# Optimization experiments

Hardware: AMD Instinct MI355X
Metric: run time of the kernel (lower is better)

Reference implementation:

```python
import jax, jax.numpy as jnp
import numpy as np

NHID = 128; NUM_CLASSES = 128; NUM_CONVS = 3; EDGE_RATIO = 0.8
B_GRAPHS = 256; N_PER_G = 256; E_PER_G = 512
N_TOTAL = B_GRAPHS * N_PER_G; E_TOTAL = B_GRAPHS * E_PER_G
ATOM_DIMS = [119, 4, 12, 12, 10, 6, 6, 2, 2]
BOND_DIMS = [5, 6, 2]


def setup_inputs():
    key = jax.random.key(0)
    ks = jax.random.split(key, 32)
    a_off = np.concatenate([[0], np.cumsum(ATOM_DIMS)[:-1]])
    x_idx = jnp.stack([jax.random.randint(ks[i], (N_TOTAL,), 0, dm) + int(o)
                       for i, (dm, o) in enumerate(zip(ATOM_DIMS, a_off))], axis=1)
    b_off = np.concatenate([[0], np.cumsum(BOND_DIMS)[:-1]])
    edge_attr_idx = jnp.stack([jax.random.randint(ks[9 + i], (E_TOTAL,), 0, dm) + int(o)
                               for i, (dm, o) in enumerate(zip(BOND_DIMS, b_off))], axis=1)
    # block-structured edges: each graph's edges are contiguous, endpoints local
    src = jax.random.randint(ks[12], (B_GRAPHS, E_PER_G), 0, N_PER_G)
    dst = jax.random.randint(ks[13], (B_GRAPHS, E_PER_G), 0, N_PER_G)
    off = jnp.arange(B_GRAPHS)[:, None] * N_PER_G
    edge_index = jnp.stack([(src + off).reshape(-1), (dst + off).reshape(-1)])
    batch = jnp.repeat(jnp.arange(B_GRAPHS), N_PER_G)
    s = 0.05
    d = NHID
    def rn(k, shape):
        return jax.random.normal(k, shape, dtype=jnp.float32) * s
    return {
        "x_idx": x_idx, "edge_attr_idx": edge_attr_idx,
        "edge_index": edge_index, "batch": batch,
        "atom_table": rn(ks[14], (sum(ATOM_DIMS), d)),
        "bond_table": rn(ks[15], (sum(BOND_DIMS), d)),
        "W_gcn": rn(ks[16], (NUM_CONVS, d, d)), "b_gcn": rn(ks[17], (NUM_CONVS, d)),
        "root_emb": rn(ks[18], (NUM_CONVS, d)),
        "W_hyp": rn(ks[19], (NUM_CONVS - 1, d, d)), "b_hyp": rn(ks[20], (NUM_CONVS - 1, d)),
        "W_sc": rn(ks[21], (NUM_CONVS - 1, d, 1)), "b_sc": rn(ks[22], (NUM_CONVS - 1, 1)),
        "Wc1": rn(ks[23], (3 * d, d)), "bc1": rn(ks[24], (d,)),
        "Wc2": rn(ks[25], (d, d // 2)), "bc2": rn(ks[26], (d // 2,)),
        "Wc3": rn(ks[27], (d // 2, NUM_CLASSES)), "bc3": rn(ks[28], (NUM_CLASSES,)),
    }


def reference(x_idx, edge_attr_idx, edge_index, batch, atom_table, bond_table,
              W_gcn, b_gcn, root_emb, W_hyp, b_hyp, W_sc, b_sc,
              Wc1, bc1, Wc2, bc2, Wc3, bc3):
    seg = jax.ops.segment_sum
    x = atom_table[x_idx].sum(axis=1)          # [N, d] AtomEncoder: sum of per-feature embeddings
    e = bond_table[edge_attr_idx].sum(axis=1)  # [E, d] BondEncoder
    edge_weight = None
    xs = 0.0
    for l in range(NUM_CONVS):
        E = edge_index.shape[1]
        # ---- DHT: dual hypergraph (edges -> nodes, nodes -> hyperedges), with loops & degree-1 mask
        flat = edge_index.T.reshape(-1)  # [2E] node ids in (src,dst,src,dst,...) order
        node_idx = jnp.concatenate([jnp.repeat(jnp.arange(E), 2), jnp.arange(E)])       # [3E]
        hyper_idx = jnp.concatenate([flat, N_TOTAL + jnp.arange(E)])                    # [3E]
        bc = seg(jnp.ones(2 * E, jnp.float32), flat, num_segments=N_TOTAL)
        mask = jnp.concatenate([bc[flat] != 1.0, jnp.ones((E,), dtype=bool)])
        w = mask.astype(x.dtype)
        NH = N_TOTAL + E
        # ---- GCNConv_OGB
        row, col = edge_index[0], edge_index[1]
        h = x @ W_gcn[l] + b_gcn[l]
        deg = seg(jnp.ones(E, x.dtype), row, num_segments=N_TOTAL) + 1.0
        dis = deg ** -0.5
        msg = (dis[row] * dis[col])[:, None] * jax.nn.relu(h[row] + e)
        if edge_weight is not None:
            msg = msg * edge_weight[:, None]
        x = jax.nn.relu(seg(msg, col, num_segments=N_TOTAL)
                        + jax.nn.relu(h + root_emb[l]) / deg[:, None])
        if l < NUM_CONVS - 1:
            # ---- HypergraphConv on edge features (nodes of dual = original edges)
            Dn = seg(w, node_idx, num_segments=E)
            Bh = seg(w, hyper_idx, num_segments=NH)
            Dinv = jnp.where(Dn > 0, 1.0 / Dn, 0.0)
            Binv = jnp.where(Bh > 0, 1.0 / Bh, 0.0)
            def hconv(feat, W, b):
                z = feat @ W
                m = seg(z[node_idx] * w[:, None], hyper_idx, num_segments=NH) * Binv[:, None]
                return seg(m[hyper_idx] * w[:, None], node_idx, num_segments=E) * Dinv[:, None] + b
            e = jax.nn.relu(hconv(e, W_hyp[l], b_hyp[l]))
            score = jnp.tanh(hconv(e, W_sc[l], b_sc[l]).squeeze(-1))  # [E]
            # ---- topk edge pooling (uniform per-graph blocks -> static k)
            Eg = E // B_GRAPHS
            k = int(np.ceil(EDGE_RATIO * Eg))
            _, loc = jax.lax.top_k(score.reshape(B_GRAPHS, Eg), k)
            perm = (loc + jnp.arange(B_GRAPHS)[:, None] * Eg).reshape(-1)
            edge_index = edge_index[:, perm]
            e = e[perm]
            edge_weight = jnp.clip(score[perm], 0.0, 1.0)
        # ---- readout: gmp | gap | gsp  (uniform graphs -> reshape)
        xr = x.reshape(B_GRAPHS, N_PER_G, NHID)
        xs = xs + jnp.concatenate([xr.max(axis=1), xr.mean(axis=1), xr.sum(axis=1)], axis=1)
    # ---- classifier (eval mode: dropout is identity)
    h1 = jax.nn.relu(xs @ Wc1 + bc1)
    h2 = jax.nn.relu(h1 @ Wc2 + bc2)
    return h2 @ Wc3 + bc3
```

## Files before the change

### kernel.cpp

```cpp
#include <hip/hip_runtime.h>
#include <hip/hip_bf16.h>
#include <math.h>

constexpr int NTOT = 65536;
constexpr int D    = 128;
constexpr int BG   = 256;
constexpr int E0 = 131072, E1 = 104960, E2 = 83968;
constexpr int EG0 = 512;
constexpr int KP0 = 410, KP1 = 328;

typedef __bf16 bf16x8 __attribute__((ext_vector_type(8)));
typedef __bf16 bf16x4 __attribute__((ext_vector_type(4)));
typedef __bf16 bf16x2 __attribute__((ext_vector_type(2)));
typedef float  f32x4  __attribute__((ext_vector_type(4)));

__device__ __forceinline__ float2 tof2(bf16x2 v) {
  return make_float2((float)v[0], (float)v[1]);
}
__device__ __forceinline__ bf16x2 tob2(float ax, float ay) {
  bf16x2 r; r[0] = (__bf16)ax; r[1] = (__bf16)ay; return r;
}

__global__ __launch_bounds__(256) void k_embed_x(const int* __restrict__ xi,
                                                 const float* __restrict__ tab,
                                                 __bf16* __restrict__ x) {
  int t = blockIdx.x * 256 + threadIdx.x;
  int v = t >> 5, q = (t & 31) << 2;
  float4 s = {0.f, 0.f, 0.f, 0.f};
#pragma unroll
  for (int j = 0; j < 9; ++j) {
    int r = xi[v * 9 + j];
    float4 a = *(const float4*)&tab[r * D + q];
    s.x += a.x; s.y += a.y; s.z += a.z; s.w += a.w;
  }
  bf16x4 o; o[0] = (__bf16)s.x; o[1] = (__bf16)s.y; o[2] = (__bf16)s.z; o[3] = (__bf16)s.w;
  *(bf16x4*)&x[(size_t)v * D + q] = o;
}

__global__ __launch_bounds__(256) void k_embed_e(const int* __restrict__ bi,
                                                 const float* __restrict__ tab,
                                                 __bf16* __restrict__ e) {
  int t = blockIdx.x * 256 + threadIdx.x;
  int i = t >> 5, q = (t & 31) << 2;
  float4 s = {0.f, 0.f, 0.f, 0.f};
#pragma unroll
  for (int j = 0; j < 3; ++j) {
    int r = bi[i * 3 + j];
    float4 a = *(const float4*)&tab[r * D + q];
    s.x += a.x; s.y += a.y; s.z += a.z; s.w += a.w;
  }
  bf16x4 o; o[0] = (__bf16)s.x; o[1] = (__bf16)s.y; o[2] = (__bf16)s.z; o[3] = (__bf16)s.w;
  *(bf16x4*)&e[(size_t)i * D + q] = o;
}

template <int EG, bool HAS_EW>
__global__ __launch_bounds__(1024, 4) void k_gcn_fused(const int* __restrict__ ei, int E,
                                                       const __bf16* __restrict__ e,
                                                       const float* __restrict__ Wg,
                                                       const float* __restrict__ bg,
                                                       const float* __restrict__ ew,
                                                       const float* __restrict__ root,
                                                       __bf16* __restrict__ x,
                                                       float* __restrict__ xs) {
  constexpr int NW = 16;
  __shared__ bf16x8 Wl[4][8][64];
  __shared__ __bf16 hl[256 * 128];
  __shared__ int   pke[EG];
  __shared__ float coef[EG];
  __shared__ int   cnts[256];
  __shared__ int   cntd[256];
  __shared__ int   off[257];
  __shared__ int   cur[256];
  __shared__ int   wsum[4];
  __shared__ short adj[EG];
  __shared__ float redm[16 * 128], reds[16 * 128];
  const int g = blockIdx.x;
  const int t = threadIdx.x, w = t >> 6, lane = t & 63;
  const bf16x2* eg2 = (const bf16x2*)e + (size_t)g * EG * 64 + lane;
  bf16x2* xg2 = (bf16x2*)x + (size_t)g * 256 * 64 + lane;

  if (t < 256) { cnts[t] = 0; cntd[t] = 0; }
  __syncthreads();

  for (int j = t; j < EG; j += 1024) {
    int s = ei[g * EG + j] & 255, d = ei[E + g * EG + j] & 255;
    pke[j] = s | (d << 8);
    atomicAdd(&cnts[s], 1);
    atomicAdd(&cntd[d], 1);
  }
  {
    bf16x8* Wf = (bf16x8*)Wl;
    for (int q = t; q < 2048; q += 1024) {
      int ks = q >> 9, nt = (q >> 6) & 7, l = q & 63;
      int kk = ks * 32 + ((l >> 4) << 3);
      int nn = nt * 16 + (l & 15);
      const float* wp = Wg + (size_t)kk * 128 + nn;
      bf16x8 v;
#pragma unroll
      for (int b = 0; b < 8; ++b) v[b] = (__bf16)wp[(size_t)b * 128];
      Wf[q] = v;
    }
  }
  __syncthreads();

  {
    const int r0 = w * 16 + (lane & 15);
    const __bf16* Ap = x + ((size_t)(g * 256 + r0)) * 128 + ((lane >> 4) << 3);
    bf16x8 af[4];
#pragma unroll
    for (int ks = 0; ks < 4; ++ks) af[ks] = *(const bf16x8*)(Ap + ks * 32);
    f32x4 acc[8] = {};
#pragma unroll
    for (int ks = 0; ks < 4; ++ks) {
#pragma unroll
      for (int nt = 0; nt < 8; ++nt) {
        acc[nt] = __builtin_amdgcn_mfma_f32_16x16x32_bf16(af[ks], Wl[ks][nt][lane], acc[nt], 0, 0, 0);
      }
    }
    const int lrow = w * 16 + ((lane >> 4) << 2);
    const int ocol = lane & 15;
#pragma unroll
    for (int nt = 0; nt < 8; ++nt) {
      float bb = bg[nt * 16 + ocol];
#pragma unroll
      for (int r = 0; r < 4; ++r)
        hl[(lrow + r) * 128 + nt * 16 + ocol] = (__bf16)(acc[nt][r] + bb);
    }
  }

  for (int j = t; j < EG; j += 1024) {
    int p = pke[j];
    int s = p & 255, d = (p >> 8) & 255;
    float c = rsqrtf(((float)cnts[s] + 1.f) * ((float)cnts[d] + 1.f));
    if (HAS_EW) c *= ew[g * EG + j];
    coef[j] = c;
  }

  {
    int v = 0;
    if (t < 256) {
      v = cntd[t];
#pragma unroll
      for (int d2 = 1; d2 < 64; d2 <<= 1) {
        int u = __shfl_up(v, d2);
        if (lane >= d2) v += u;
      }
      if (lane == 63) wsum[w] = v;
    }
    __syncthreads();
    if (t < 256) {
      int add = 0;
      if (w > 0) add += wsum[0];
      if (w > 1) add += wsum[1];
      if (w > 2) add += wsum[2];
      off[t + 1] = v + add;
      if (t == 0) off[0] = 0;
      cur[t] = v + add - cntd[t];
    }
    __syncthreads();
  }

  for (int j = t; j < EG; j += 1024) {
    int d = (pke[j] >> 8) & 255;
    int pos = atomicAdd(&cur[d], 1);
    adj[pos] = (short)j;
  }
  __syncthreads();

  const float rvx = root[2 * lane], rvy = root[2 * lane + 1];
  float2 mx = {-1e30f, -1e30f}, sm = {0.f, 0.f};
  for (int n = w; n < 256; n += NW) {
    float2 val = {0.f, 0.f};
    int b0 = off[n], b1 = off[n + 1];
    int k = b0;
    for (; k + 1 < b1; k += 2) {
      int j0 = adj[k], j1 = adj[k + 1];
      int s0 = pke[j0] & 255, s1 = pke[j1] & 255;
      float2 e0 = tof2(eg2[(size_t)j0 * 64]), e1 = tof2(eg2[(size_t)j1 * 64]);
      float2 h0 = tof2(*(const bf16x2*)&hl[s0 * 128 + 2 * lane]);
      float2 h1 = tof2(*(const bf16x2*)&hl[s1 * 128 + 2 * lane]);
      float c0 = coef[j0], c1 = coef[j1];
      val.x += c0 * fmaxf(h0.x + e0.x, 0.f) + c1 * fmaxf(h1.x + e1.x, 0.f);
      val.y += c0 * fmaxf(h0.y + e0.y, 0.f) + c1 * fmaxf(h1.y + e1.y, 0.f);
    }
    if (k < b1) {
      int j0 = adj[k];
      int s0 = pke[j0] & 255;
      float2 e0 = tof2(eg2[(size_t)j0 * 64]);
      float2 h0 = tof2(*(const bf16x2*)&hl[s0 * 128 + 2 * lane]);
      float c0 = coef[j0];
      val.x += c0 * fmaxf(h0.x + e0.x, 0.f);
      val.y += c0 * fmaxf(h0.y + e0.y, 0.f);
    }
    float inv = 1.f / ((float)cnts[n] + 1.f);
    float2 hv = tof2(*(const bf16x2*)&hl[n * 128 + 2 * lane]);
    float xvx = fmaxf(val.x + fmaxf(hv.x + rvx, 0.f) * inv, 0.f);
    float xvy = fmaxf(val.y + fmaxf(hv.y + rvy, 0.f) * inv, 0.f);
    xg2[(size_t)n * 64] = tob2(xvx, xvy);
    mx.x = fmaxf(mx.x, xvx); mx.y = fmaxf(mx.y, xvy);
    sm.x += xvx;             sm.y += xvy;
  }
  redm[w * 128 + 2 * lane]     = mx.x;
  redm[w * 128 + 2 * lane + 1] = mx.y;
  reds[w * 128 + 2 * lane]     = sm.x;
  reds[w * 128 + 2 * lane + 1] = sm.y;
  __syncthreads();

  if (t < 128) {
    float M = redm[t], S2 = reds[t];
#pragma unroll
    for (int k = 1; k < 16; ++k) {
      M = fmaxf(M, redm[k * 128 + t]);
      S2 += reds[k * 128 + t];
    }
    xs[g * 384 + t]       += M;
    xs[g * 384 + 128 + t] += S2 * (1.f / 256.f);
    xs[g * 384 + 256 + t] += S2;
  }
}

template <int EG, int KEEP, int ENEW>
__global__ __launch_bounds__(1024, 4) void k_hyper_sort(const int* __restrict__ ei, int E,
                                                        __bf16* __restrict__ e,
                                                        const float* __restrict__ Wh,
                                                        const float* __restrict__ bias,
                                                        const float* __restrict__ wsc,
                                                        const float* __restrict__ bsc,
                                                        __bf16* __restrict__ zbuf,
                                                        int* __restrict__ ei_new,
                                                        __bf16* __restrict__ e_new,
                                                        float* __restrict__ ew) {
  constexpr int NW = 16;
  __shared__ bf16x8 Wl[4][8][64];
  __shared__ __bf16 S[256 * 128];
  __shared__ int   pke[EG];
  __shared__ float as_[EG], ad_[EG], az_[EG];
  __shared__ float zsh[EG];
  __shared__ float Ssh[256];
  __shared__ int   cnt[256];
  __shared__ int   off[257];
  __shared__ int   cur[256];
  __shared__ int   wsum[4];
  __shared__ short adj[2 * EG];
  __shared__ float ls[512];
  __shared__ int   li[512];
  __shared__ int   sidx[512];
  const int g = blockIdx.x;
  const int t = threadIdx.x, w = t >> 6, lane = t & 63;
  const bf16x2* zg2 = (const bf16x2*)zbuf + (size_t)g * EG * 64 + lane;
  bf16x2* eo2 = (bf16x2*)e + (size_t)g * EG * 64 + lane;
  bf16x2* S2 = (bf16x2*)S;

  if (t < 256) { cnt[t] = 0; Ssh[t] = 0.f; }
  __syncthreads();

  for (int j = t; j < EG; j += 1024) {
    int s = ei[g * EG + j] & 255, d = ei[E + g * EG + j] & 255;
    pke[j] = s | (d << 8);
    atomicAdd(&cnt[s], 1);
    atomicAdd(&cnt[d], 1);
  }
  {
    bf16x8* Wf = (bf16x8*)Wl;
    for (int q = t; q < 2048; q += 1024) {
      int ks = q >> 9, nt = (q >> 6) & 7, l = q & 63;
      int kk = ks * 32 + ((l >> 4) << 3);
      int nn = nt * 16 + (l & 15);
      const float* wp = Wh + (size_t)kk * 128 + nn;
      bf16x8 v;
#pragma unroll
      for (int b = 0; b < 8; ++b) v[b] = (__bf16)wp[(size_t)b * 128];
      Wf[q] = v;
    }
  }
  const int r0 = w * 32 + (lane & 15);
  const int r1 = r0 + 16;
  bf16x8 a0[4], a1[4];
  {
    bf16x8 zz = {};
    const __bf16* Ap0 = e + ((size_t)g * EG + r0) * 128 + ((lane >> 4) << 3);
    const __bf16* Ap1 = Ap0 + (size_t)16 * 128;
#pragma unroll
    for (int ks = 0; ks < 4; ++ks) {
      a0[ks] = (r0 < EG) ? *(const bf16x8*)(Ap0 + ks * 32) : zz;
      a1[ks] = (r1 < EG) ? *(const bf16x8*)(Ap1 + ks * 32) : zz;
    }
  }
  __syncthreads();

  {
    f32x4 acc0[8] = {}; f32x4 acc1[8] = {};
#pragma unroll
    for (int ks = 0; ks < 4; ++ks) {
#pragma unroll
      for (int nt = 0; nt < 8; ++nt) {
        bf16x8 b = Wl[ks][nt][lane];
        acc0[nt] = __builtin_amdgcn_mfma_f32_16x16x32_bf16(a0[ks], b, acc0[nt], 0, 0, 0);
        acc1[nt] = __builtin_amdgcn_mfma_f32_16x16x32_bf16(a1[ks], b, acc1[nt], 0, 0, 0);
      }
    }
    const int orow = w * 32 + ((lane >> 4) << 2);
    const int ocol = lane & 15;
#pragma unroll
    for (int nt = 0; nt < 8; ++nt) {
      __bf16* zp = zbuf + ((size_t)g * EG + orow) * 128 + nt * 16 + ocol;
#pragma unroll
      for (int r = 0; r < 4; ++r) {
        if (orow + r < EG)      zp[(size_t)r * 128]        = (__bf16)acc0[nt][r];
        if (orow + 16 + r < EG) zp[(size_t)(16 + r) * 128] = (__bf16)acc1[nt][r];
      }
    }
  }

  for (int j = t; j < EG; j += 1024) {
    int p = pke[j];
    int s = p & 255, d = (p >> 8) & 255;
    int cs = cnt[s], cd = cnt[d];
    float bis  = (cs != 1) ? 1.f / (float)cs : 0.f;
    float bid_ = (cd != 1) ? 1.f / (float)cd : 0.f;
    float dinv = 1.f / (1.f + (cs != 1 ? 1.f : 0.f) + (cd != 1 ? 1.f : 0.f));
    as_[j] = dinv * bis;
    ad_[j] = dinv * bid_;
    az_[j] = dinv;
  }

  {
    int v = 0;
    if (t < 256) {
      v = cnt[t];
#pragma unroll
      for (int d2 = 1; d2 < 64; d2 <<= 1) {
        int u = __shfl_up(v, d2);
        if (lane >= d2) v += u;
      }
      if (lane == 63) wsum[w] = v;
    }
    __syncthreads();
    if (t < 256) {
      int add = 0;
      if (w > 0) add += wsum[0];
      if (w > 1) add += wsum[1];
      if (w > 2) add += wsum[2];
      off[t + 1] = v + add;
      if (t == 0) off[0] = 0;
      cur[t] = v + add - cnt[t];
    }
    __syncthreads();
  }

  for (int j = t; j < EG; j += 1024) {
    int p = pke[j];
    int pos0 = atomicAdd(&cur[p & 255], 1);
    adj[pos0] = (short)j;
    int pos1 = atomicAdd(&cur[(p >> 8) & 255], 1);
    adj[pos1] = (short)j;
  }
  __syncthreads();

  for (int n = w; n < 256; n += NW) {
    float2 val = {0.f, 0.f};
    int b0 = off[n], b1 = off[n + 1];
    int k = b0;
    for (; k + 1 < b1; k += 2) {
      float2 a = tof2(zg2[(size_t)adj[k] * 64]);
      float2 b = tof2(zg2[(size_t)adj[k + 1] * 64]);
      val.x += a.x + b.x;
      val.y += a.y + b.y;
    }
    if (k < b1) {
      float2 a = tof2(zg2[(size_t)adj[k] * 64]);
      val.x += a.x; val.y += a.y;
    }
    S2[n * 64 + lane] = tob2(val.x, val.y);
  }
  __syncthreads();

  const float bbx = bias[2 * lane], bby = bias[2 * lane + 1];
  const float wvx = wsc[2 * lane],  wvy = wsc[2 * lane + 1];
  for (int j = w; j < EG; j += NW) {
    int p = pke[j];
    int s = p & 255, d = (p >> 8) & 255;
    float a_s = as_[j], a_d = ad_[j], a_z = az_[j];
    float2 Sv = tof2(S2[s * 64 + lane]);
    float2 Dv = tof2(S2[d * 64 + lane]);
    float2 zv = tof2(zg2[(size_t)j * 64]);
    float ox = fmaxf(a_s * Sv.x + a_d * Dv.x + a_z * zv.x + bbx, 0.f);
    float oy = fmaxf(a_s * Sv.y + a_d * Dv.y + a_z * zv.y + bby, 0.f);
    eo2[(size_t)j * 64] = tob2(ox, oy);
    float part = ox * wvx + oy * wvy;
#pragma unroll
    for (int offs = 32; offs > 0; offs >>= 1) part += __shfl_xor(part, offs);
    if (lane == 0) zsh[j] = part;
  }
  __syncthreads();

  if (t < EG) {
    float v = zsh[t];
    atomicAdd(&Ssh[pke[t] & 255], v);
    atomicAdd(&Ssh[(pke[t] >> 8) & 255], v);
  }
  __syncthreads();

  float sc = -INFINITY; int idx = 0x7FFFFFFF;
  if (t < EG) {
    int p = pke[t];
    int sn = p & 255, dn = (p >> 8) & 255;
    sc = tanhf(as_[t] * Ssh[sn] + ad_[t] * Ssh[dn] + az_[t] * zsh[t] + bsc[0]);
    idx = t;
  }
#pragma unroll
  for (int k = 2; k <= 512; k <<= 1) {
#pragma unroll
    for (int j = k >> 1; j > 0; j >>= 1) {
      if (j < 64) {
        if (t < 512) {
          float ps = __shfl_xor(sc, j);
          int   pi = __shfl_xor(idx, j);
          bool ownBetter = (sc > ps) || (sc == ps && idx < pi);
          bool lower = ((t & j) == 0);
          bool desc = ((t & k) == 0);
          bool keep = desc ? (lower ? ownBetter : !ownBetter)
                           : (lower ? !ownBetter : ownBetter);
          if (!keep) { sc = ps; idx = pi; }
        }
      } else {
        if (t < 512) { ls[t] = sc; li[t] = idx; }
        __syncthreads();
        if (t < 512) {
          float ps = ls[t ^ j];
          int   pi = li[t ^ j];
          bool ownBetter = (sc > ps) || (sc == ps && idx < pi);
          bool lower = ((t & j) == 0);
          bool desc = ((t & k) == 0);
          bool keep = desc ? (lower ? ownBetter : !ownBetter)
                           : (lower ? !ownBetter : ownBetter);
          if (!keep) { sc = ps; idx = pi; }
        }
        __syncthreads();
      }
    }
  }

  if (t < 512) sidx[t] = idx;
  if (t < KEEP) {
    int oldp = g * EG + idx;
    int newp = g * KEEP + t;
    ei_new[newp]        = ei[oldp];
    ei_new[ENEW + newp] = ei[E + oldp];
    ew[newp] = fminf(fmaxf(sc, 0.f), 1.f);
  }
  __syncthreads();

  const float4* src = (const float4*)e;
  float4* dst = (float4*)e_new;
  for (int q = t; q < KEEP * 16; q += 1024) {
    int j2 = q >> 4, c = q & 15;
    dst[((size_t)g * KEEP + j2) * 16 + c] = src[((size_t)g * EG + sidx[j2]) * 16 + c];
  }
}

__global__ __launch_bounds__(128) void k_mlp(const float* __restrict__ xs,
                                             const float* __restrict__ Wc1, const float* __restrict__ bc1,
                                             const float* __restrict__ Wc2, const float* __restrict__ bc2,
                                             const float* __restrict__ Wc3, const float* __restrict__ bc3,
                                             float* __restrict__ out) {
  __shared__ float row[384];
  __shared__ float h1[128];
  __shared__ float h2[64];
  int g = blockIdx.x, t = threadIdx.x;
  for (int i = t; i < 384; i += 128) row[i] = xs[g * 384 + i];
  __syncthreads();
  float a = bc1[t];
  for (int k = 0; k < 384; ++k) a += row[k] * Wc1[k * 128 + t];
  h1[t] = fmaxf(a, 0.f);
  __syncthreads();
  if (t < 64) {
    float b = bc2[t];
    for (int k = 0; k < 128; ++k) b += h1[k] * Wc2[k * 64 + t];
    h2[t] = fmaxf(b, 0.f);
  }
  __syncthreads();
  float o = bc3[t];
  for (int k = 0; k < 64; ++k) o += h2[k] * Wc3[k * 128 + t];
  out[g * 128 + t] = o;
}

extern "C" void kernel_launch(void* const* d_in, const int* in_sizes, int n_in,
                              void* d_out, int out_size, void* d_ws, size_t ws_size,
                              hipStream_t stream) {
  (void)in_sizes; (void)n_in; (void)out_size; (void)ws_size;
  const int*   x_idx  = (const int*)d_in[0];
  const int*   b_idx  = (const int*)d_in[1];
  const int*   ei0    = (const int*)d_in[2];
  const float* atom_t = (const float*)d_in[4];
  const float* bond_t = (const float*)d_in[5];
  const float* W_gcn  = (const float*)d_in[6];
  const float* b_gcn  = (const float*)d_in[7];
  const float* root   = (const float*)d_in[8];
  const float* W_hyp  = (const float*)d_in[9];
  const float* b_hyp  = (const float*)d_in[10];
  const float* W_sc   = (const float*)d_in[11];
  const float* b_sc   = (const float*)d_in[12];
  const float* Wc1    = (const float*)d_in[13];
  const float* bc1_   = (const float*)d_in[14];
  const float* Wc2    = (const float*)d_in[15];
  const float* bc2_   = (const float*)d_in[16];
  const float* Wc3    = (const float*)d_in[17];
  const float* bc3_   = (const float*)d_in[18];
  float* out = (float*)d_out;

  __bf16* x    = (__bf16*)d_ws;
  __bf16* eA   = x    + (size_t)NTOT * D;
  __bf16* eB   = eA   + (size_t)E0 * D;
  __bf16* zbuf = eB   + (size_t)E0 * D;
  float* ew  = (float*)(zbuf + (size_t)E0 * D);
  float* xs  = ew + E0;
  int*   eiB  = (int*)(xs + BG * 384);
  int*   eiA2 = eiB + 2 * E0;

  hipMemsetAsync(xs, 0, BG * 384 * 4, stream);
  k_embed_x<<<NTOT * 32 / 256, 256, 0, stream>>>(x_idx, atom_t, x);
  k_embed_e<<<E0 * 32 / 256, 256, 0, stream>>>(b_idx, bond_t, eA);

  k_gcn_fused<EG0, false><<<BG, 1024, 0, stream>>>(ei0, E0, eA, W_gcn, b_gcn, nullptr, root, x, xs);
  k_hyper_sort<EG0, KP0, E1><<<BG, 1024, 0, stream>>>(ei0, E0, eA, W_hyp, b_hyp, W_sc, b_sc, zbuf, eiB, eB, ew);

  k_gcn_fused<KP0, true><<<BG, 1024, 0, stream>>>(eiB, E1, eB, W_gcn + D * D, b_gcn + D, ew, root + D, x, xs);
  k_hyper_sort<KP0, KP1, E2><<<BG, 1024, 0, stream>>>(eiB, E1, eB, W_hyp + D * D, b_hyp + D, W_sc + D, b_sc + 1, zbuf, eiA2, eA, ew);

  k_gcn_fused<KP1, true><<<BG, 1024, 0, stream>>>(eiA2, E2, eA, W_gcn + 2 * D * D, b_gcn + 2 * D, ew, root + 2 * D, x, xs);

  k_mlp<<<BG, 128, 0, stream>>>(xs, Wc1, bc1_, Wc2, bc2_, Wc3, bc3_, out);
}
```

Measured before the change: 225.1 us.

## Aggregate raw edge features before matmul and drop global z buffer

Reorders the hyperedge conv so per-node sums are taken over raw edge features e instead of z = e@W, using linearity: (sum e)@W is done once on the 256 node rows in shared memory. The per-edge matmul is then fused into the epilogue, where bias, ReLU, the writeback and the score dot product are computed straight from MFMA accumulators. This removes the global zbuf write and its re-reads. The trade-off is a second small MFMA pass over the shared node tile and scattered LDS reads of the node rows indexed by src/dst, plus more register pressure in the epilogue.

Result: no change. 224.3 us (-0.3%).

```diff
diff --git a/kernel.cpp b/kernel.cpp
--- a/kernel.cpp
+++ b/kernel.cpp
@@ -226,13 +226,12 @@
                                                         const float* __restrict__ bias,
                                                         const float* __restrict__ wsc,
                                                         const float* __restrict__ bsc,
-                                                        __bf16* __restrict__ zbuf,
                                                         int* __restrict__ ei_new,
                                                         __bf16* __restrict__ e_new,
                                                         float* __restrict__ ew) {
   constexpr int NW = 16;
   __shared__ bf16x8 Wl[4][8][64];
-  __shared__ __bf16 S[256 * 128];
+  __shared__ __bf16 ES[256 * 128];
   __shared__ int   pke[EG];
   __shared__ float as_[EG], ad_[EG], az_[EG];
   __shared__ float zsh[EG];
@@ -247,9 +246,9 @@
   __shared__ int   sidx[512];
   const int g = blockIdx.x;
   const int t = threadIdx.x, w = t >> 6, lane = t & 63;
-  const bf16x2* zg2 = (const bf16x2*)zbuf + (size_t)g * EG * 64 + lane;
-  bf16x2* eo2 = (bf16x2*)e + (size_t)g * EG * 64 + lane;
-  bf16x2* S2 = (bf16x2*)S;
+  const int hi = lane >> 4, lo = lane & 15;
+  const bf16x2* eg2 = (const bf16x2*)e + (size_t)g * EG * 64 + lane;
+  bf16x2* ES2 = (bf16x2*)ES;
 
   if (t < 256) { cnt[t] = 0; Ssh[t] = 0.f; }
   __syncthreads();
@@ -273,44 +272,7 @@
       Wf[q] = v;
     }
   }
-  const int r0 = w * 32 + (lane & 15);
-  const int r1 = r0 + 16;
-  bf16x8 a0[4], a1[4];
-  {
-    bf16x8 zz = {};
-    const __bf16* Ap0 = e + ((size_t)g * EG + r0) * 128 + ((lane >> 4) << 3);
-    const __bf16* Ap1 = Ap0 + (size_t)16 * 128;
-#pragma unroll
-    for (int ks = 0; ks < 4; ++ks) {
-      a0[ks] = (r0 < EG) ? *(const bf16x8*)(Ap0 + ks * 32) : zz;
-      a1[ks] = (r1 < EG) ? *(const bf16x8*)(Ap1 + ks * 32) : zz;
-    }
-  }
-  __syncthreads();
-
-  {
-    f32x4 acc0[8] = {}; f32x4 acc1[8] = {};
-#pragma unroll
-    for (int ks = 0; ks < 4; ++ks) {
-#pragma unroll
-      for (int nt = 0; nt < 8; ++nt) {
-        bf16x8 b = Wl[ks][nt][lane];
-        acc0[nt] = __builtin_amdgcn_mfma_f32_16x16x32_bf16(a0[ks], b, acc0[nt], 0, 0, 0);
-        acc1[nt] = __builtin_amdgcn_mfma_f32_16x16x32_bf16(a1[ks], b, acc1[nt], 0, 0, 0);
-      }
-    }
-    const int orow = w * 32 + ((lane >> 4) << 2);
-    const int ocol = lane & 15;
-#pragma unroll
-    for (int nt = 0; nt < 8; ++nt) {
-      __bf16* zp = zbuf + ((size_t)g * EG + orow) * 128 + nt * 16 + ocol;
-#pragma unroll
-      for (int r = 0; r < 4; ++r) {
-        if (orow + r < EG)      zp[(size_t)r * 128]        = (__bf16)acc0[nt][r];
-        if (orow + 16 + r < EG) zp[(size_t)(16 + r) * 128] = (__bf16)acc1[nt][r];
-      }
-    }
-  }
+  __syncthreads();
 
   for (int j = t; j < EG; j += 1024) {
     int p = pke[j];
@@ -362,35 +324,128 @@
     int b0 = off[n], b1 = off[n + 1];
     int k = b0;
     for (; k + 1 < b1; k += 2) {
-      float2 a = tof2(zg2[(size_t)adj[k] * 64]);
-      float2 b = tof2(zg2[(size_t)adj[k + 1] * 64]);
+      float2 a = tof2(eg2[(size_t)adj[k] * 64]);
+      float2 b = tof2(eg2[(size_t)adj[k + 1] * 64]);
       val.x += a.x + b.x;
       val.y += a.y + b.y;
     }
     if (k < b1) {
-      float2 a = tof2(zg2[(size_t)adj[k] * 64]);
+      float2 a = tof2(eg2[(size_t)adj[k] * 64]);
       val.x += a.x; val.y += a.y;
     }
-    S2[n * 64 + lane] = tob2(val.x, val.y);
-  }
-  __syncthreads();
-
-  const float bbx = bias[2 * lane], bby = bias[2 * lane + 1];
-  const float wvx = wsc[2 * lane],  wvy = wsc[2 * lane + 1];
-  for (int j = w; j < EG; j += NW) {
-    int p = pke[j];
-    int s = p & 255, d = (p >> 8) & 255;
-    float a_s = as_[j], a_d = ad_[j], a_z = az_[j];
-    float2 Sv = tof2(S2[s * 64 + lane]);
-    float2 Dv = tof2(S2[d * 64 + lane]);
-    float2 zv = tof2(zg2[(size_t)j * 64]);
-    float ox = fmaxf(a_s * Sv.x + a_d * Dv.x + a_z * zv.x + bbx, 0.f);
-    float oy = fmaxf(a_s * Sv.y + a_d * Dv.y + a_z * zv.y + bby, 0.f);
-    eo2[(size_t)j * 64] = tob2(ox, oy);
-    float part = ox * wvx + oy * wvy;
-#pragma unroll
-    for (int offs = 32; offs > 0; offs >>= 1) part += __shfl_xor(part, offs);
-    if (lane == 0) zsh[j] = part;
+    ES2[n * 64 + lane] = tob2(val.x, val.y);
+  }
+  __syncthreads();
+
+  {
+    const int mr = w * 16 + lo;
+    const __bf16* Ep = ES + mr * 128 + (hi << 3);
+    bf16x8 ef[4];
+#pragma unroll
+    for (int ks = 0; ks < 4; ++ks) ef[ks] = *(const bf16x8*)(Ep + ks * 32);
+    f32x4 acc[8] = {};
+#pragma unroll
+    for (int ks = 0; ks < 4; ++ks) {
+#pragma unroll
+      for (int nt = 0; nt < 8; ++nt) {
+        acc[nt] = __builtin_amdgcn_mfma_f32_16x16x32_bf16(ef[ks], Wl[ks][nt][lane], acc[nt], 0, 0, 0);
+      }
+    }
+    const int lrow = w * 16 + (hi << 2);
+#pragma unroll
+    for (int nt = 0; nt < 8; ++nt) {
+#pragma unroll
+      for (int r = 0; r < 4; ++r)
+        ES[(lrow + r) * 128 + nt * 16 + lo] = (__bf16)acc[nt][r];
+    }
+  }
+  __syncthreads();
+
+  {
+    const int r0 = w * 32 + lo;
+    const int r1 = r0 + 16;
+    bf16x8 a0[4], a1[4];
+    {
+      bf16x8 zz = {};
+      const __bf16* Ap0 = e + ((size_t)g * EG + r0) * 128 + (hi << 3);
+      const __bf16* Ap1 = Ap0 + (size_t)16 * 128;
+#pragma unroll
+      for (int ks = 0; ks < 4; ++ks) {
+        a0[ks] = (r0 < EG) ? *(const bf16x8*)(Ap0 + ks * 32) : zz;
+        a1[ks] = (r1 < EG) ? *(const bf16x8*)(Ap1 + ks * 32) : zz;
+      }
+    }
+    f32x4 acc0[8] = {}; f32x4 acc1[8] = {};
+#pragma unroll
+    for (int ks = 0; ks < 4; ++ks) {
+#pragma unroll
+      for (int nt = 0; nt < 8; ++nt) {
+        bf16x8 b = Wl[ks][nt][lane];
+        acc0[nt] = __builtin_amdgcn_mfma_f32_16x16x32_bf16(a0[ks], b, acc0[nt], 0, 0, 0);
+        acc1[nt] = __builtin_amdgcn_mfma_f32_16x16x32_bf16(a1[ks], b, acc1[nt], 0, 0, 0);
+      }
+    }
+    const int row0 = w * 32 + (hi << 2);
+    const int row1 = row0 + 16;
+    float wv[8], bb[8];
+#pragma unroll
+    for (int nt = 0; nt < 8; ++nt) {
+      wv[nt] = wsc[nt * 16 + lo];
+      bb[nt] = bias[nt * 16 + lo];
+    }
+    float as0[4], ad0[4], az0[4], as1[4], ad1[4], az1[4];
+    int ps0[4], pd0[4], ps1[4], pd1[4];
+#pragma unroll
+    for (int r = 0; r < 4; ++r) {
+      int ra = row0 + r;
+      if (ra < EG) {
+        int p = pke[ra];
+        ps0[r] = (p & 255) * 128; pd0[r] = ((p >> 8) & 255) * 128;
+        as0[r] = as_[ra]; ad0[r] = ad_[ra]; az0[r] = az_[ra];
+      } else { ps0[r] = 0; pd0[r] = 0; as0[r] = 0.f; ad0[r] = 0.f; az0[r] = 0.f; }
+      int rb = row1 + r;
+      if (rb < EG) {
+        int p = pke[rb];
+        ps1[r] = (p & 255) * 128; pd1[r] = ((p >> 8) & 255) * 128;
+        as1[r] = as_[rb]; ad1[r] = ad_[rb]; az1[r] = az_[rb];
+      } else { ps1[r] = 0; pd1[r] = 0; as1[r] = 0.f; ad1[r] = 0.f; az1[r] = 0.f; }
+    }
+    float sp0[4] = {0.f, 0.f, 0.f, 0.f};
+    float sp1[4] = {0.f, 0.f, 0.f, 0.f};
+#pragma unroll
+    for (int nt = 0; nt < 8; ++nt) {
+      int col = nt * 16 + lo;
+#pragma unroll
+      for (int r = 0; r < 4; ++r) {
+        if (row0 + r < EG) {
+          float o = fmaxf(as0[r] * (float)ES[ps0[r] + col] + ad0[r] * (float)ES[pd0[r] + col]
+                          + az0[r] * acc0[nt][r] + bb[nt], 0.f);
+          e[((size_t)g * EG + row0 + r) * 128 + col] = (__bf16)o;
+          sp0[r] += o * wv[nt];
+        }
+        if (row1 + r < EG) {
+          float o = fmaxf(as1[r] * (float)ES[ps1[r] + col] + ad1[r] * (float)ES[pd1[r] + col]
+                          + az1[r] * acc1[nt][r] + bb[nt], 0.f);
+          e[((size_t)g * EG + row1 + r) * 128 + col] = (__bf16)o;
+          sp1[r] += o * wv[nt];
+        }
+      }
+    }
+#pragma unroll
+    for (int offs = 1; offs < 16; offs <<= 1) {
+#pragma unroll
+      for (int r = 0; r < 4; ++r) {
+        sp0[r] += __shfl_xor(sp0[r], offs);
+        sp1[r] += __shfl_xor(sp1[r], offs);
+      }
+    }
+    if (lo == 0) {
+#pragma unroll
+      for (int r = 0; r < 4; ++r) {
+        if (row0 + r < EG) zsh[row0 + r] = sp0[r];
+        if (row1 + r < EG) zsh[row1 + r] = sp1[r];
+      }
+    }
   }
   __syncthreads();
 
@@ -512,8 +567,7 @@
   __bf16* x    = (__bf16*)d_ws;
   __bf16* eA   = x    + (size_t)NTOT * D;
   __bf16* eB   = eA   + (size_t)E0 * D;
-  __bf16* zbuf = eB   + (size_t)E0 * D;
-  float* ew  = (float*)(zbuf + (size_t)E0 * D);
+  float* ew  = (float*)(eB + (size_t)E0 * D);
   float* xs  = ew + E0;
   int*   eiB  = (int*)(xs + BG * 384);
   int*   eiA2 = eiB + 2 * E0;
@@ -523,10 +577,10 @@
   k_embed_e<<<E0 * 32 / 256, 256, 0, stream>>>(b_idx, bond_t, eA);
 
   k_gcn_fused<EG0, false><<<BG, 1024, 0, stream>>>(ei0, E0, eA, W_gcn, b_gcn, nullptr, root, x, xs);
-  k_hyper_sort<EG0, KP0, E1><<<BG, 1024, 0, stream>>>(ei0, E0, eA, W_hyp, b_hyp, W_sc, b_sc, zbuf, eiB, eB, ew);
+  k_hyper_sort<EG0, KP0, E1><<<BG, 1024, 0, stream>>>(ei0, E0, eA, W_hyp, b_hyp, W_sc, b_sc, eiB, eB, ew);
 
   k_gcn_fused<KP0, true><<<BG, 1024, 0, stream>>>(eiB, E1, eB, W_gcn + D * D, b_gcn + D, ew, root + D, x, xs);
-  k_hyper_sort<KP0, KP1, E2><<<BG, 1024, 0, stream>>>(eiB, E1, eB, W_hyp + D * D, b_hyp + D, W_sc + D, b_sc + 1, zbuf, eiA2, eA, ew);
+  k_hyper_sort<KP0, KP1, E2><<<BG, 1024, 0, stream>>>(eiB, E1, eB, W_hyp + D * D, b_hyp + D, W_sc + D, b_sc + 1, eiA2, eA, ew);
 
   k_gcn_fused<KP1, true><<<BG, 1024, 0, stream>>>(eiA2, E2, eA, W_gcn + 2 * D * D, b_gcn + 2 * D, ew, root + 2 * D, x, xs);
 
```
